# Performance work log

Hardware: AMD Instinct MI355X
Metric: run time of the kernel (lower is better)

## Reference

```python
import jax, jax.numpy as jnp
import numpy as np
from itertools import permutations

SIZES = (16, 32, 32, 32)  # token_sizes for layout dims (v, t, h, w)
N = SIZES[0] * SIZES[1] * SIZES[2] * SIZES[3]  # num_tokens = 524288
B = 32
EPS = 1e-3


def setup_inputs() -> dict:
    key = jax.random.key(0)
    ks = jax.random.split(key, 12)
    u = lambda k, shape: jax.random.uniform(k, shape, dtype=jnp.float32)
    alphas = [1.0, 2.0, 4.0]
    comps = np.array(
        [[alphas[v], alphas[t], alphas[hw], alphas[hw]]
         for v, t, hw in permutations(range(3), 3)], dtype=np.float32)  # [6, 4]
    return {
        "components": jnp.asarray(comps),
        "u_rate_src": u(ks[0], (1,)),
        "u_rate_tgt": u(ks[1], (1,)),
        "u0_src": u(ks[2], (B, N)),
        "u0_tgt": u(ks[3], (B, N)),
        "u_v_src": u(ks[4], (B, SIZES[0])),
        "u_t_src": u(ks[5], (B, SIZES[1])),
        "u_h_src": u(ks[6], (B, SIZES[2])),
        "u_w_src": u(ks[7], (B, SIZES[3])),
        "u_v_tgt": u(ks[8], (B, SIZES[0])),
        "u_t_tgt": u(ks[9], (B, SIZES[1])),
        "u_h_tgt": u(ks[10], (B, SIZES[2])),
        "u_w_tgt": u(ks[11], (B, SIZES[3])),
        "idx": 2,
    }


def _clamp(x):
    return jnp.clip(x, EPS, 1.0 - EPS)


def _binary_mask(u_rate, u0, u_dims, alphas):
    # event_prior: log-prob per token = log U0 + sum_dim log(U_dim)/alpha_dim (broadcast over pattern)
    P = jnp.log(_clamp(u0))  # [B, N]
    for i, ud in enumerate(u_dims):
        shape = [B, 1, 1, 1, 1]
        shape[1 + i] = SIZES[i]
        rep = jnp.broadcast_to(
            (jnp.log(_clamp(ud)) / alphas[i]).reshape(shape),
            (B,) + SIZES).reshape(B, N)
        P = P + rep
    # rate_prior: one shared uniform, K = floor(U * N), expanded over batch
    K = (_clamp(u_rate) * N).astype(jnp.int32)  # [1]
    K = jnp.broadcast_to(K, (B,))[:, None]  # [B, 1]
    # binary_topk_: rank via double argsort (0 = largest), mask = K > rank
    rank = jnp.argsort(jnp.argsort(-P, axis=-1), axis=-1)
    return K > rank


def reference(components, u_rate_src, u_rate_tgt, u0_src, u0_tgt,
              u_v_src, u_t_src, u_h_src, u_w_src,
              u_v_tgt, u_t_tgt, u_h_tgt, u_w_tgt, idx):
    alphas = components[idx]  # [4], one alpha per layout dim, shared by src/tgt
    src = _binary_mask(u_rate_src, u0_src,
                       (u_v_src, u_t_src, u_h_src, u_w_src), alphas)
    tgt = _binary_mask(u_rate_tgt, u0_tgt,
                       (u_v_tgt, u_t_tgt, u_h_tgt, u_w_tgt), alphas)
    return src, tgt
```

## Files before the change

### kernel.cpp

```cpp
#include <hip/hip_runtime.h>
#include <stdint.h>

#define NTOK 524288
#define ROWS 64
#define CHUNKS 64
#define NTHR 256
#define F4_PER_ROW (NTOK / 4)
#define F4_PER_CHUNK (F4_PER_ROW / CHUNKS)
#define F4_PER_THR (F4_PER_CHUNK / NTHR)
#define NB1 2048
#define B1BASE 30720
#define BCAP 65536
#define GCAP 8192
#define STAGECAP 512

#define OFF_H16  0u
#define OFF_B1   (OFF_H16 + ROWS * NB1 * 4u)
#define OFF_CG   (OFF_B1 + 256u)
#define OFF_BCNT (OFF_CG + 256u)
#define OFF_IT   (OFF_BCNT + 256u)
#define OFF_T    (OFF_IT + 256u)
#define OFF_ZERO_END (OFF_T + 512u)
#define OFF_TAB  OFF_ZERO_END
#define OFF_BK   (OFF_TAB + ROWS * 112u * 8u)
#define OFF_BI   (OFF_BK + (size_t)ROWS * BCAP * 8u)

__device__ __forceinline__ double clamp64(double x) {
  return fmin(fmax(x, 1.0e-3), 1.0 - 1.0e-3);
}

__device__ __forceinline__ unsigned compute_K(float ur) {
  float urf = fminf(fmaxf(ur, 1.0e-3f), 1.0f - 1.0e-3f);
  return (unsigned)(int)(urf * (float)NTOK);
}

__device__ __forceinline__ int bucket16(unsigned long long kb) {
  int b = (int)(unsigned)(kb >> 47) - B1BASE;
  return b < 0 ? 0 : (b > NB1 - 1 ? NB1 - 1 : b);
}

__global__ void k_tables(const float* __restrict__ comps, const int* __restrict__ idxp,
                         const float* __restrict__ uvs, const float* __restrict__ uts,
                         const float* __restrict__ uhs, const float* __restrict__ uws,
                         const float* __restrict__ uvt, const float* __restrict__ utt,
                         const float* __restrict__ uht, const float* __restrict__ uwt,
                         double* __restrict__ tabs) {
  int idx = idxp[0];
  double alpha[4];
  for (int d = 0; d < 4; ++d) alpha[d] = (double)comps[idx * 4 + d];
  for (int i = threadIdx.x; i < ROWS * 112; i += blockDim.x) {
    int row = i / 112, j = i % 112;
    int m = row >> 5, b = row & 31;
    int d, jj, dsz;
    if (j < 16)      { d = 0; jj = j;      dsz = 16; }
    else if (j < 48) { d = 1; jj = j - 16; dsz = 32; }
    else if (j < 80) { d = 2; jj = j - 48; dsz = 32; }
    else             { d = 3; jj = j - 80; dsz = 32; }
    const float* u;
    if (m == 0) u = (d == 0) ? uvs : (d == 1) ? uts : (d == 2) ? uhs : uws;
    else        u = (d == 0) ? uvt : (d == 1) ? utt : (d == 2) ? uht : uwt;
    double x = clamp64((double)u[b * dsz + jj]);
    double a = alpha[d];
    double f;
    if (a == 1.0)      f = x;
    else if (a == 2.0) f = sqrt(x);
    else if (a == 4.0) f = sqrt(sqrt(x));
    else               f = pow(x, 1.0 / a);
    tabs[row * 112 + j] = f;
  }
}

__global__ void k_hist16(const float* __restrict__ u0s, const float* __restrict__ u0t,
                         const double* __restrict__ tabs, unsigned int* __restrict__ h16) {
  __shared__ double tb[112];
  __shared__ unsigned int h[NB1];
  int row = blockIdx.x / CHUNKS, chunk = blockIdx.x % CHUNKS;
  for (int i = threadIdx.x; i < 112; i += blockDim.x) tb[i] = tabs[row * 112 + i];
  for (int i = threadIdx.x; i < NB1; i += blockDim.x) h[i] = 0;
  __syncthreads();
  int m = row >> 5, b = row & 31;
  const float4* u0 = reinterpret_cast<const float4*>((m ? u0t : u0s) + (size_t)b * NTOK);
  int base = chunk * F4_PER_CHUNK;
  for (int it = 0; it < F4_PER_THR; ++it) {
    int f4 = base + it * NTHR + threadIdx.x;
    float4 x = u0[f4];
    int n0 = f4 * 4;
    int w0 = n0 & 31, hh = (n0 >> 5) & 31, tt = (n0 >> 10) & 31, vv = n0 >> 15;
    double g = tb[vv] * tb[16 + tt] * tb[48 + hh];
    double k0 = clamp64((double)x.x) * (g * tb[80 + w0 + 0]);
    double k1 = clamp64((double)x.y) * (g * tb[80 + w0 + 1]);
    double k2 = clamp64((double)x.z) * (g * tb[80 + w0 + 2]);
    double k3 = clamp64((double)x.w) * (g * tb[80 + w0 + 3]);
    atomicAdd(&h[bucket16((unsigned long long)__double_as_longlong(k0))], 1u);
    atomicAdd(&h[bucket16((unsigned long long)__double_as_longlong(k1))], 1u);
    atomicAdd(&h[bucket16((unsigned long long)__double_as_longlong(k2))], 1u);
    atomicAdd(&h[bucket16((unsigned long long)__double_as_longlong(k3))], 1u);
  }
  __syncthreads();
  for (int i = threadIdx.x; i < NB1; i += blockDim.x) {
    unsigned c = h[i];
    if (c) atomicAdd(&h16[row * NB1 + i], c);
  }
}

__global__ __launch_bounds__(256) void k_scan16(const unsigned int* __restrict__ h16,
                                                const float* __restrict__ urs,
                                                const float* __restrict__ urt,
                                                int* __restrict__ sB1, int* __restrict__ sCG) {
  __shared__ unsigned suf[256];
  __shared__ int best;
  int row = blockIdx.x;
  int t = threadIdx.x;
  const unsigned* h = h16 + row * NB1;
  unsigned loc[8]; unsigned own = 0;
#pragma unroll
  for (int i = 0; i < 8; ++i) { loc[i] = h[t * 8 + i]; own += loc[i]; }
  suf[t] = own;
  if (t == 0) best = -1;
  __syncthreads();
  for (int off = 1; off < 256; off <<= 1) {
    unsigned add = (t + off < 256) ? suf[t + off] : 0u;
    __syncthreads();
    suf[t] += add;
    __syncthreads();
  }
  int m = row >> 5;
  unsigned K = compute_K(m ? urt[0] : urs[0]);
  unsigned above = suf[t] - own;
  int cand = -1;
  unsigned cum = above;
  for (int i = 7; i >= 0; --i) {
    if (cum + loc[i] >= K) { cand = t * 8 + i; break; }
    cum += loc[i];
  }
  if (cand >= 0) atomicMax(&best, cand);
  __syncthreads();
  int bb = best;
  if (bb >= 0 && (bb >> 3) == t) {
    unsigned cg = above;
    for (int i = 7; i > (bb & 7); --i) cg += loc[i];
    sB1[row] = bb;
    sCG[row] = (int)cg;
  }
}

__global__ void k_gather2(const float* __restrict__ u0s, const float* __restrict__ u0t,
                          const double* __restrict__ tabs, const int* __restrict__ sB1,
                          unsigned int* __restrict__ bcnt,
                          unsigned long long* __restrict__ bk, unsigned int* __restrict__ bi) {
  __shared__ double tb[112];
  __shared__ unsigned long long sk[STAGECAP];
  __shared__ unsigned int si[STAGECAP];
  __shared__ unsigned int scnt, sbase;
  int row = blockIdx.x / CHUNKS, chunk = blockIdx.x % CHUNKS;
  for (int i = threadIdx.x; i < 112; i += blockDim.x) tb[i] = tabs[row * 112 + i];
  if (threadIdx.x == 0) scnt = 0;
  __syncthreads();
  int b1 = sB1[row];
  int m = row >> 5, b = row & 31;
  const float4* u0 = reinterpret_cast<const float4*>((m ? u0t : u0s) + (size_t)b * NTOK);
  int base = chunk * F4_PER_CHUNK;
  for (int it = 0; it < F4_PER_THR; ++it) {
    int f4 = base + it * NTHR + threadIdx.x;
    float4 x = u0[f4];
    int n0 = f4 * 4;
    int w0 = n0 & 31, hh = (n0 >> 5) & 31, tt = (n0 >> 10) & 31, vv = n0 >> 15;
    double g = tb[vv] * tb[16 + tt] * tb[48 + hh];
    double ks[4];
    ks[0] = clamp64((double)x.x) * (g * tb[80 + w0 + 0]);
    ks[1] = clamp64((double)x.y) * (g * tb[80 + w0 + 1]);
    ks[2] = clamp64((double)x.z) * (g * tb[80 + w0 + 2]);
    ks[3] = clamp64((double)x.w) * (g * tb[80 + w0 + 3]);
#pragma unroll
    for (int c = 0; c < 4; ++c) {
      unsigned long long kb = (unsigned long long)__double_as_longlong(ks[c]);
      if (bucket16(kb) == b1) {
        unsigned p = atomicAdd(&scnt, 1u);
        if (p < STAGECAP) { sk[p] = kb; si[p] = (unsigned)(n0 + c); }
        else {
          unsigned gp = atomicAdd(&bcnt[row], 1u);
          if (gp < BCAP) {
            bk[(size_t)row * BCAP + gp] = kb;
            bi[(size_t)row * BCAP + gp] = (unsigned)(n0 + c);
          }
        }
      }
    }
  }
  __syncthreads();
  unsigned nst = scnt; if (nst > STAGECAP) nst = STAGECAP;
  if (threadIdx.x == 0) sbase = atomicAdd(&bcnt[row], nst);
  __syncthreads();
  unsigned bs = sbase;
  for (unsigned i = threadIdx.x; i < nst; i += blockDim.x) {
    unsigned gp = bs + i;
    if (gp < BCAP) {
      bk[(size_t)row * BCAP + gp] = sk[i];
      bi[(size_t)row * BCAP + gp] = si[i];
    }
  }
}

__global__ __launch_bounds__(256) void k_pick(const unsigned long long* __restrict__ bk,
                                              const unsigned int* __restrict__ bi,
                                              const unsigned int* __restrict__ bcnt,
                                              const float* __restrict__ urs,
                                              const float* __restrict__ urt,
                                              const int* __restrict__ sCG,
                                              unsigned long long* __restrict__ sT,
                                              int* __restrict__ sIT) {
  __shared__ unsigned int h[4096];
  __shared__ unsigned suf[256];
  __shared__ int best;
  __shared__ unsigned long long kk[GCAP];
  __shared__ unsigned int ixx[GCAP];
  __shared__ unsigned int lcnt;
  int row = blockIdx.x;
  int t = threadIdx.x;
  unsigned cnt = bcnt[row]; if (cnt > BCAP) cnt = BCAP;
  const unsigned long long* rbk = bk + (size_t)row * BCAP;
  const unsigned int* rbi = bi + (size_t)row * BCAP;
  for (int i = t; i < 4096; i += 256) h[i] = 0;
  if (t == 0) { best = -1; lcnt = 0; }
  __syncthreads();
  for (unsigned i = t; i < cnt; i += 256)
    atomicAdd(&h[(unsigned)(rbk[i] >> 39) & 0xFFFu], 1u);
  __syncthreads();
  unsigned loc[16]; unsigned own = 0;
#pragma unroll
  for (int i = 0; i < 16; ++i) { loc[i] = h[t * 16 + i]; own += loc[i]; }
  suf[t] = own;
  __syncthreads();
  for (int off = 1; off < 256; off <<= 1) {
    unsigned add = (t + off < 256) ? suf[t + off] : 0u;
    __syncthreads();
    suf[t] += add;
    __syncthreads();
  }
  int m = row >> 5;
  unsigned K = compute_K(m ? urt[0] : urs[0]);
  unsigned K2 = K - (unsigned)sCG[row];
  unsigned above = suf[t] - own;
  int cand = -1;
  unsigned cum = above;
  for (int i = 15; i >= 0; --i) {
    if (cum + loc[i] >= K2) { cand = t * 16 + i; break; }
    cum += loc[i];
  }
  if (cand >= 0) atomicMax(&best, cand);
  __syncthreads();
  int b2 = best;
  __shared__ unsigned sharedRem;
  if (b2 >= 0 && (b2 >> 4) == t) {
    unsigned a2 = above;
    for (int i = 15; i > (b2 & 15); --i) a2 += loc[i];
    sharedRem = K2 - a2;
  }
  __syncthreads();
  unsigned rem = sharedRem;
  for (unsigned i = t; i < cnt; i += 256) {
    unsigned long long kb = rbk[i];
    if (((unsigned)(kb >> 39) & 0xFFFu) == (unsigned)b2) {
      unsigned p = atomicAdd(&lcnt, 1u);
      if (p < GCAP) { kk[p] = kb; ixx[p] = rbi[i]; }
    }
  }
  __syncthreads();
  unsigned n_r = lcnt; if (n_r > GCAP) n_r = GCAP;
  unsigned n2 = 2;
  while (n2 < n_r) n2 <<= 1;
  for (unsigned i = t; i < n2; i += 256)
    if (i >= n_r) { kk[i] = 0ULL; ixx[i] = 0xFFFFFFFFu; }
  __syncthreads();
  for (unsigned kstep = 2; kstep <= n2; kstep <<= 1) {
    for (unsigned j = kstep >> 1; j > 0; j >>= 1) {
      for (int i = t; i < (int)n2; i += 256) {
        int pj = i ^ (int)j;
        if (pj > i) {
          unsigned long long k1 = kk[i], k2v = kk[pj];
          unsigned i1 = ixx[i], i2 = ixx[pj];
          bool bef = (k1 > k2v) || (k1 == k2v && i1 < i2);
          bool dirAsc = ((i & (int)kstep) == 0);
          if (bef != dirAsc) { kk[i] = k2v; kk[pj] = k1; ixx[i] = i2; ixx[pj] = i1; }
        }
      }
      __syncthreads();
    }
  }
  if (t == 0) {
    int r = (int)rem;
    if (r < 1) r = 1;
    if ((unsigned)r > n_r) r = (int)n_r;
    sT[row] = kk[r - 1];
    sIT[row] = (int)ixx[r - 1];
  }
}

__global__ void k_final(const float* __restrict__ u0s, const float* __restrict__ u0t,
                        const double* __restrict__ tabs,
                        const unsigned long long* __restrict__ sT, const int* __restrict__ sIT,
                        int* __restrict__ out) {
  __shared__ double tb[112];
  int row = blockIdx.x / CHUNKS, chunk = blockIdx.x % CHUNKS;
  for (int i = threadIdx.x; i < 112; i += blockDim.x) tb[i] = tabs[row * 112 + i];
  __syncthreads();
  unsigned long long T = sT[row];
  int IT = sIT[row];
  int m = row >> 5, b = row & 31;
  const float4* u0 = reinterpret_cast<const float4*>((m ? u0t : u0s) + (size_t)b * NTOK);
  int4* o = reinterpret_cast<int4*>(out + (size_t)row * NTOK);
  int base = chunk * F4_PER_CHUNK;
  for (int it = 0; it < F4_PER_THR; ++it) {
    int f4 = base + it * NTHR + threadIdx.x;
    float4 x = u0[f4];
    int n0 = f4 * 4;
    int w0 = n0 & 31, hh = (n0 >> 5) & 31, tt = (n0 >> 10) & 31, vv = n0 >> 15;
    double g = tb[vv] * tb[16 + tt] * tb[48 + hh];
    unsigned long long kb0 = (unsigned long long)__double_as_longlong(clamp64((double)x.x) * (g * tb[80 + w0 + 0]));
    unsigned long long kb1 = (unsigned long long)__double_as_longlong(clamp64((double)x.y) * (g * tb[80 + w0 + 1]));
    unsigned long long kb2 = (unsigned long long)__double_as_longlong(clamp64((double)x.z) * (g * tb[80 + w0 + 2]));
    unsigned long long kb3 = (unsigned long long)__double_as_longlong(clamp64((double)x.w) * (g * tb[80 + w0 + 3]));
    int4 r;
    r.x = (kb0 > T || (kb0 == T && (n0 + 0) <= IT)) ? 1 : 0;
    r.y = (kb1 > T || (kb1 == T && (n0 + 1) <= IT)) ? 1 : 0;
    r.z = (kb2 > T || (kb2 == T && (n0 + 2) <= IT)) ? 1 : 0;
    r.w = (kb3 > T || (kb3 == T && (n0 + 3) <= IT)) ? 1 : 0;
    o[f4] = r;
  }
}

extern "C" void kernel_launch(void* const* d_in, const int* in_sizes, int n_in,
                              void* d_out, int out_size, void* d_ws, size_t ws_size,
                              hipStream_t stream) {
  const float* comps = (const float*)d_in[0];
  const float* urs   = (const float*)d_in[1];
  const float* urt   = (const float*)d_in[2];
  const float* u0s   = (const float*)d_in[3];
  const float* u0t   = (const float*)d_in[4];
  const float* uvs   = (const float*)d_in[5];
  const float* uts   = (const float*)d_in[6];
  const float* uhs   = (const float*)d_in[7];
  const float* uws   = (const float*)d_in[8];
  const float* uvt   = (const float*)d_in[9];
  const float* utt   = (const float*)d_in[10];
  const float* uht   = (const float*)d_in[11];
  const float* uwt   = (const float*)d_in[12];
  const int*   idxp  = (const int*)d_in[13];
  int* out = (int*)d_out;

  char* ws = (char*)d_ws;
  unsigned int*       h16  = (unsigned int*)(ws + OFF_H16);
  int*                sB1  = (int*)(ws + OFF_B1);
  int*                sCG  = (int*)(ws + OFF_CG);
  unsigned int*       bcnt = (unsigned int*)(ws + OFF_BCNT);
  int*                sIT  = (int*)(ws + OFF_IT);
  unsigned long long* sT   = (unsigned long long*)(ws + OFF_T);
  double*             tabs = (double*)(ws + OFF_TAB);
  unsigned long long* bk   = (unsigned long long*)(ws + OFF_BK);
  unsigned int*       bi   = (unsigned int*)(ws + OFF_BI);

  hipMemsetAsync(d_ws, 0, OFF_ZERO_END, stream);

  k_tables<<<1, 256, 0, stream>>>(comps, idxp, uvs, uts, uhs, uws, uvt, utt, uht, uwt, tabs);
  k_hist16<<<ROWS * CHUNKS, NTHR, 0, stream>>>(u0s, u0t, tabs, h16);
  k_scan16<<<ROWS, 256, 0, stream>>>(h16, urs, urt, sB1, sCG);
  k_gather2<<<ROWS * CHUNKS, NTHR, 0, stream>>>(u0s, u0t, tabs, sB1, bcnt, bk, bi);
  k_pick<<<ROWS, 256, 0, stream>>>(bk, bi, bcnt, urs, urt, sCG, sT, sIT);
  k_final<<<ROWS * CHUNKS, NTHR, 0, stream>>>(u0s, u0t, tabs, sT, sIT, out);
}
```

Measured before the change: 368.4 us.

## Write mask during gather pass and fix up boundary bucket only

The gather kernel now writes the output mask directly, marking tokens whose bucket lies above the threshold bucket as selected. A small per-row fixup kernel then resolves only the candidates in the threshold bucket, using the final key and index threshold. This drops the full third pass over the u0 input and its key recomputation. Separately, the histogram kernel now uses half as many chunks per row, so each thread does twice the work. The trade is a scattered write pattern in the fixup kernel and a full output write inside the gather pass.

New measurement: 342.2 us. 1.08x faster.

```diff
diff --git a/kernel.cpp b/kernel.cpp
--- a/kernel.cpp
+++ b/kernel.cpp
@@ -4,10 +4,13 @@
 #define NTOK 524288
 #define ROWS 64
 #define CHUNKS 64
+#define CHUNKS_H 32
 #define NTHR 256
 #define F4_PER_ROW (NTOK / 4)
 #define F4_PER_CHUNK (F4_PER_ROW / CHUNKS)
 #define F4_PER_THR (F4_PER_CHUNK / NTHR)
+#define F4_PER_CHUNK_H (F4_PER_ROW / CHUNKS_H)
+#define F4_PER_THR_H (F4_PER_CHUNK_H / NTHR)
 #define NB1 2048
 #define B1BASE 30720
 #define BCAP 65536
@@ -74,14 +77,14 @@
                          const double* __restrict__ tabs, unsigned int* __restrict__ h16) {
   __shared__ double tb[112];
   __shared__ unsigned int h[NB1];
-  int row = blockIdx.x / CHUNKS, chunk = blockIdx.x % CHUNKS;
+  int row = blockIdx.x / CHUNKS_H, chunk = blockIdx.x % CHUNKS_H;
   for (int i = threadIdx.x; i < 112; i += blockDim.x) tb[i] = tabs[row * 112 + i];
   for (int i = threadIdx.x; i < NB1; i += blockDim.x) h[i] = 0;
   __syncthreads();
   int m = row >> 5, b = row & 31;
   const float4* u0 = reinterpret_cast<const float4*>((m ? u0t : u0s) + (size_t)b * NTOK);
-  int base = chunk * F4_PER_CHUNK;
-  for (int it = 0; it < F4_PER_THR; ++it) {
+  int base = chunk * F4_PER_CHUNK_H;
+  for (int it = 0; it < F4_PER_THR_H; ++it) {
     int f4 = base + it * NTHR + threadIdx.x;
     float4 x = u0[f4];
     int n0 = f4 * 4;
@@ -144,10 +147,11 @@
   }
 }
 
-__global__ void k_gather2(const float* __restrict__ u0s, const float* __restrict__ u0t,
+__global__ void k_gatherw(const float* __restrict__ u0s, const float* __restrict__ u0t,
                           const double* __restrict__ tabs, const int* __restrict__ sB1,
                           unsigned int* __restrict__ bcnt,
-                          unsigned long long* __restrict__ bk, unsigned int* __restrict__ bi) {
+                          unsigned long long* __restrict__ bk, unsigned int* __restrict__ bi,
+                          int* __restrict__ out) {
   __shared__ double tb[112];
   __shared__ unsigned long long sk[STAGECAP];
   __shared__ unsigned int si[STAGECAP];
@@ -159,6 +163,7 @@
   int b1 = sB1[row];
   int m = row >> 5, b = row & 31;
   const float4* u0 = reinterpret_cast<const float4*>((m ? u0t : u0s) + (size_t)b * NTOK);
+  int4* o = reinterpret_cast<int4*>(out + (size_t)row * NTOK);
   int base = chunk * F4_PER_CHUNK;
   for (int it = 0; it < F4_PER_THR; ++it) {
     int f4 = base + it * NTHR + threadIdx.x;
@@ -171,10 +176,13 @@
     ks[1] = clamp64((double)x.y) * (g * tb[80 + w0 + 1]);
     ks[2] = clamp64((double)x.z) * (g * tb[80 + w0 + 2]);
     ks[3] = clamp64((double)x.w) * (g * tb[80 + w0 + 3]);
+    int r[4];
 #pragma unroll
     for (int c = 0; c < 4; ++c) {
       unsigned long long kb = (unsigned long long)__double_as_longlong(ks[c]);
-      if (bucket16(kb) == b1) {
+      int bkt = bucket16(kb);
+      r[c] = (bkt > b1) ? 1 : 0;
+      if (bkt == b1) {
         unsigned p = atomicAdd(&scnt, 1u);
         if (p < STAGECAP) { sk[p] = kb; si[p] = (unsigned)(n0 + c); }
         else {
@@ -186,6 +194,8 @@
         }
       }
     }
+    int4 rv; rv.x = r[0]; rv.y = r[1]; rv.z = r[2]; rv.w = r[3];
+    o[f4] = rv;
   }
   __syncthreads();
   unsigned nst = scnt; if (nst > STAGECAP) nst = STAGECAP;
@@ -215,6 +225,7 @@
   __shared__ unsigned long long kk[GCAP];
   __shared__ unsigned int ixx[GCAP];
   __shared__ unsigned int lcnt;
+  __shared__ unsigned sharedRem;
   int row = blockIdx.x;
   int t = threadIdx.x;
   unsigned cnt = bcnt[row]; if (cnt > BCAP) cnt = BCAP;
@@ -250,7 +261,6 @@
   if (cand >= 0) atomicMax(&best, cand);
   __syncthreads();
   int b2 = best;
-  __shared__ unsigned sharedRem;
   if (b2 >= 0 && (b2 >> 4) == t) {
     unsigned a2 = above;
     for (int i = 15; i > (b2 & 15); --i) a2 += loc[i];
@@ -296,36 +306,23 @@
   }
 }
 
-__global__ void k_final(const float* __restrict__ u0s, const float* __restrict__ u0t,
-                        const double* __restrict__ tabs,
-                        const unsigned long long* __restrict__ sT, const int* __restrict__ sIT,
-                        int* __restrict__ out) {
-  __shared__ double tb[112];
-  int row = blockIdx.x / CHUNKS, chunk = blockIdx.x % CHUNKS;
-  for (int i = threadIdx.x; i < 112; i += blockDim.x) tb[i] = tabs[row * 112 + i];
-  __syncthreads();
+__global__ __launch_bounds__(256) void k_fixup(const unsigned long long* __restrict__ bk,
+                                               const unsigned int* __restrict__ bi,
+                                               const unsigned int* __restrict__ bcnt,
+                                               const unsigned long long* __restrict__ sT,
+                                               const int* __restrict__ sIT,
+                                               int* __restrict__ out) {
+  int row = blockIdx.x;
+  unsigned cnt = bcnt[row]; if (cnt > BCAP) cnt = BCAP;
   unsigned long long T = sT[row];
   int IT = sIT[row];
-  int m = row >> 5, b = row & 31;
-  const float4* u0 = reinterpret_cast<const float4*>((m ? u0t : u0s) + (size_t)b * NTOK);
-  int4* o = reinterpret_cast<int4*>(out + (size_t)row * NTOK);
-  int base = chunk * F4_PER_CHUNK;
-  for (int it = 0; it < F4_PER_THR; ++it) {
-    int f4 = base + it * NTHR + threadIdx.x;
-    float4 x = u0[f4];
-    int n0 = f4 * 4;
-    int w0 = n0 & 31, hh = (n0 >> 5) & 31, tt = (n0 >> 10) & 31, vv = n0 >> 15;
-    double g = tb[vv] * tb[16 + tt] * tb[48 + hh];
-    unsigned long long kb0 = (unsigned long long)__double_as_longlong(clamp64((double)x.x) * (g * tb[80 + w0 + 0]));
-    unsigned long long kb1 = (unsigned long long)__double_as_longlong(clamp64((double)x.y) * (g * tb[80 + w0 + 1]));
-    unsigned long long kb2 = (unsigned long long)__double_as_longlong(clamp64((double)x.z) * (g * tb[80 + w0 + 2]));
-    unsigned long long kb3 = (unsigned long long)__double_as_longlong(clamp64((double)x.w) * (g * tb[80 + w0 + 3]));
-    int4 r;
-    r.x = (kb0 > T || (kb0 == T && (n0 + 0) <= IT)) ? 1 : 0;
-    r.y = (kb1 > T || (kb1 == T && (n0 + 1) <= IT)) ? 1 : 0;
-    r.z = (kb2 > T || (kb2 == T && (n0 + 2) <= IT)) ? 1 : 0;
-    r.w = (kb3 > T || (kb3 == T && (n0 + 3) <= IT)) ? 1 : 0;
-    o[f4] = r;
+  const unsigned long long* rbk = bk + (size_t)row * BCAP;
+  const unsigned int* rbi = bi + (size_t)row * BCAP;
+  int* o = out + (size_t)row * NTOK;
+  for (unsigned i = threadIdx.x; i < cnt; i += blockDim.x) {
+    unsigned long long kb = rbk[i];
+    unsigned idx = rbi[i];
+    o[idx] = (kb > T || (kb == T && (int)idx <= IT)) ? 1 : 0;
   }
 }
 
@@ -362,9 +359,9 @@
   hipMemsetAsync(d_ws, 0, OFF_ZERO_END, stream);
 
   k_tables<<<1, 256, 0, stream>>>(comps, idxp, uvs, uts, uhs, uws, uvt, utt, uht, uwt, tabs);
-  k_hist16<<<ROWS * CHUNKS, NTHR, 0, stream>>>(u0s, u0t, tabs, h16);
+  k_hist16<<<ROWS * CHUNKS_H, NTHR, 0, stream>>>(u0s, u0t, tabs, h16);
   k_scan16<<<ROWS, 256, 0, stream>>>(h16, urs, urt, sB1, sCG);
-  k_gather2<<<ROWS * CHUNKS, NTHR, 0, stream>>>(u0s, u0t, tabs, sB1, bcnt, bk, bi);
+  k_gatherw<<<ROWS * CHUNKS, NTHR, 0, stream>>>(u0s, u0t, tabs, sB1, bcnt, bk, bi, out);
   k_pick<<<ROWS, 256, 0, stream>>>(bk, bi, bcnt, urs, urt, sCG, sT, sIT);
-  k_final<<<ROWS * CHUNKS, NTHR, 0, stream>>>(u0s, u0t, tabs, sT, sIT, out);
-}
+  k_fixup<<<ROWS, 256, 0, stream>>>(bk, bi, bcnt, sT, sIT, out);
+}
```
